# Performance work log

Measured on AMD Instinct MI355X. Metric: run time of the kernel, lower is better.

The kernel has to match this reference:

```python
import jax, jax.numpy as jnp
import numpy as np

N, T, S, E, H, DFF = 4, 2048, 2048, 512, 8, 2048
DH = E // H
EPS = 1e-5


def layer_norm(x, w, b):
    m = jnp.mean(x, axis=-1, keepdims=True)
    v = jnp.mean(jnp.square(x - m), axis=-1, keepdims=True)
    return (x - m) * jax.lax.rsqrt(v + EPS) * w + b


def mha(q, k, v, wq, bq, wk, bk, wv, bv, wo, bo, mask=None):
    # q: (N,Tq,E), k/v: (N,Tk,E); torch Linear convention: y = x @ W.T + b
    Nq, Tq, _ = q.shape
    Tk = k.shape[1]
    Q = (q @ wq.T + bq).reshape(Nq, Tq, H, DH).transpose(0, 2, 1, 3)  # (N,H,Tq,DH)
    K = (k @ wk.T + bk).reshape(Nq, Tk, H, DH).transpose(0, 2, 1, 3)
    V = (v @ wv.T + bv).reshape(Nq, Tk, H, DH).transpose(0, 2, 1, 3)
    scores = jnp.einsum('bhtd,bhsd->bhts', Q, K) * (1.0 / np.sqrt(DH))  # (N,H,Tq,Tk)
    if mask is not None:
        scores = jnp.where(mask, scores, jnp.float32(-1e9))
    attn = jax.nn.softmax(scores, axis=-1)
    out = jnp.einsum('bhts,bhsd->bhtd', attn, V)  # (N,H,Tq,DH)
    out = out.transpose(0, 2, 1, 3).reshape(Nq, Tq, E)
    return out @ wo.T + bo


def setup_inputs() -> dict:
    key = jax.random.key(0)
    ks = jax.random.split(key, 20)
    s = 0.02

    def lin(k, out_d, in_d):
        return jax.random.normal(k, (out_d, in_d), jnp.float32) * s

    inp = {
        'tgt': jax.random.normal(ks[0], (N, T, E), jnp.float32),
        'memory': jax.random.normal(ks[1], (N, S, E), jnp.float32),
        'tgt_mask': jnp.tril(jnp.ones((T, T), dtype=bool)),  # causal (T,T)
        # self-attention params
        'sa_wq': lin(ks[2], E, E), 'sa_bq': jnp.zeros((E,), jnp.float32),
        'sa_wk': lin(ks[3], E, E), 'sa_bk': jnp.zeros((E,), jnp.float32),
        'sa_wv': lin(ks[4], E, E), 'sa_bv': jnp.zeros((E,), jnp.float32),
        'sa_wo': lin(ks[5], E, E), 'sa_bo': jnp.zeros((E,), jnp.float32),
        # cross-attention params
        'ca_wq': lin(ks[6], E, E), 'ca_bq': jnp.zeros((E,), jnp.float32),
        'ca_wk': lin(ks[7], E, E), 'ca_bk': jnp.zeros((E,), jnp.float32),
        'ca_wv': lin(ks[8], E, E), 'ca_bv': jnp.zeros((E,), jnp.float32),
        'ca_wo': lin(ks[9], E, E), 'ca_bo': jnp.zeros((E,), jnp.float32),
        # FFN params
        'w1': lin(ks[10], DFF, E), 'b1': jnp.zeros((DFF,), jnp.float32),
        'w2': lin(ks[11], E, DFF), 'b2': jnp.zeros((E,), jnp.float32),
        # LayerNorm params
        'ln1_w': jnp.ones((E,), jnp.float32), 'ln1_b': jnp.zeros((E,), jnp.float32),
        'ln2_w': jnp.ones((E,), jnp.float32), 'ln2_b': jnp.zeros((E,), jnp.float32),
        'ln3_w': jnp.ones((E,), jnp.float32), 'ln3_b': jnp.zeros((E,), jnp.float32),
    }
    return inp


def reference(tgt, memory, tgt_mask,
              sa_wq, sa_bq, sa_wk, sa_bk, sa_wv, sa_bv, sa_wo, sa_bo,
              ca_wq, ca_bq, ca_wk, ca_bk, ca_wv, ca_bv, ca_wo, ca_bo,
              w1, b1, w2, b2,
              ln1_w, ln1_b, ln2_w, ln2_b, ln3_w, ln3_b):
    # stage 1: masked self-attention + residual + LN (dropout=0 / eval mode)
    sa = mha(tgt, tgt, tgt, sa_wq, sa_bq, sa_wk, sa_bk, sa_wv, sa_bv, sa_wo, sa_bo, mask=tgt_mask)
    x = layer_norm(tgt + sa, ln1_w, ln1_b)
    # stage 2: cross-attention over encoder memory + residual + LN
    ca = mha(x, memory, memory, ca_wq, ca_bq, ca_wk, ca_bk, ca_wv, ca_bv, ca_wo, ca_bo)
    x = layer_norm(x + ca, ln2_w, ln2_b)
    # stage 3: FFN (ReLU) + residual + LN
    mlp = jax.nn.relu(x @ w1.T + b1) @ w2.T + b2
    out = layer_norm(x + mlp, ln3_w, ln3_b)
    return out
```

## Files before the change

### kernel.cpp

```cpp
#include <hip/hip_runtime.h>
#include <hip/hip_bf16.h>
#include <cstdint>

typedef short short8 __attribute__((ext_vector_type(8)));
typedef short short4v __attribute__((ext_vector_type(4)));
typedef float f32x4 __attribute__((ext_vector_type(4)));
typedef float f32x16 __attribute__((ext_vector_type(16)));

#define GLL16(gp, lp) __builtin_amdgcn_global_load_lds( \
    (const __attribute__((address_space(1))) unsigned int*)(gp), \
    (__attribute__((address_space(3))) unsigned int*)(lp), 16, 0, 0)

__device__ __forceinline__ float bf2f(ushort u) {
    union { unsigned int i; float f; } v; v.i = ((unsigned int)u) << 16; return v.f;
}
__device__ __forceinline__ ushort f2bf(float f) {
    union { float f; unsigned int u; } v; v.f = f;
    unsigned int r = v.u + 0x7FFFu + ((v.u >> 16) & 1u);
    return (ushort)(r >> 16);
}
__device__ __forceinline__ int cvtpk_bf16(float lo, float hi) {
    int r;
    asm("v_cvt_pk_bf16_f32 %0, %1, %2" : "=v"(r) : "v"(lo), "v"(hi));
    return r;
}
__device__ __forceinline__ void plane32_swap(int& a, int& b) {
    asm volatile("v_permlane32_swap_b32 %0, %1" : "+v"(a), "+v"(b));
}

struct CvtArgs {
    const float* src[12];
    ushort*      dst[12];
};
__global__ __launch_bounds__(256) void f2b_all(CvtArgs a)
{
    int id = blockIdx.x;
    int seg, boff;
    if (id < 4096)       { seg = 0; boff = id; }
    else if (id < 8192)  { seg = 1; boff = id - 4096; }
    else if (id < 10240) { int t = id - 8192; seg = 2 + (t >> 8); boff = t & 255; }
    else if (id < 11264) { seg = 10; boff = id - 10240; }
    else                 { seg = 11; boff = id - 11264; }
    int i = (boff * 256 + threadIdx.x) * 4;
    f32x4 v = *(const f32x4*)(a.src[seg] + i);
    short4v o;
#pragma unroll
    for (int e = 0; e < 4; ++e) o[e] = (short)f2bf(v[e]);
    *(short4v*)(a.dst[seg] + i) = o;
}

template<int MODE, int DEPTH>
__global__ __launch_bounds__(256) void gemm_bt(
    const ushort* __restrict__ A, const ushort* __restrict__ W,
    const float* __restrict__ b0, const float* __restrict__ b1,
    const float* __restrict__ b2,
    ushort* __restrict__ C0, ushort* __restrict__ C1, ushort* __restrict__ C2,
    int M, int N, int K)
{
    __shared__ ushort As[DEPTH][128 * 32];
    __shared__ ushort Bs[DEPTH][128 * 32];
    const int tid = threadIdx.x;
    const int l  = tid & 63;
    const int w  = tid >> 6;
    const int wr = w >> 1, wc = w & 1;
    const int bn = blockIdx.x, bm = blockIdx.y;
    const int lg = l >> 4, li = l & 15;

    const ushort* Ab = A + (size_t)(bm * 128) * K;
    const ushort* Bb = W + (size_t)(bn * 128) * K;

    f32x4 acc[4][4] = {};

    const int r0 = tid >> 2,         s0 = (tid & 3) ^ ((r0 >> 2) & 3);
    const int r1 = (tid + 256) >> 2, s1 = (tid & 3) ^ ((r1 >> 2) & 3);

    auto stage = [&](int buf, int kt) {
        const ushort* Ak = Ab + kt * 32;
        const ushort* Bk = Bb + kt * 32;
        GLL16(Ak + (size_t)r0 * K + s0 * 8, &As[buf][tid * 8]);
        GLL16(Ak + (size_t)r1 * K + s1 * 8, &As[buf][(tid + 256) * 8]);
        GLL16(Bk + (size_t)r0 * K + s0 * 8, &Bs[buf][tid * 8]);
        GLL16(Bk + (size_t)r1 * K + s1 * 8, &Bs[buf][(tid + 256) * 8]);
    };

    const int nk = K >> 5;
#pragma unroll
    for (int p = 0; p < DEPTH - 1; ++p)
        if (p < nk) stage(p, p);

    for (int kt = 0; kt < nk; ++kt) {
        const int b = kt & (DEPTH - 1);
        const int nxt = kt + DEPTH - 1;
        if (nxt < nk) stage(nxt & (DEPTH - 1), nxt);
        const int rem = nk - 1 - kt;
        const int fl = rem < DEPTH - 1 ? rem : DEPTH - 1;
        if (fl >= 3)      asm volatile("s_waitcnt vmcnt(12)" ::: "memory");
        else if (fl == 2) asm volatile("s_waitcnt vmcnt(8)"  ::: "memory");
        else if (fl == 1) asm volatile("s_waitcnt vmcnt(4)"  ::: "memory");
        else              asm volatile("s_waitcnt vmcnt(0)"  ::: "memory");
        __builtin_amdgcn_s_barrier();
        __builtin_amdgcn_sched_barrier(0);

        short8 af[4], bfr[4];
#pragma unroll
        for (int mi = 0; mi < 4; ++mi) {
            int row = wr * 64 + mi * 16 + li;
            int ch  = lg ^ ((row >> 2) & 3);
            af[mi] = *(const short8*)(&As[b][row * 32 + ch * 8]);
        }
#pragma unroll
        for (int ni = 0; ni < 4; ++ni) {
            int row = wc * 64 + ni * 16 + li;
            int ch  = lg ^ ((row >> 2) & 3);
            bfr[ni] = *(const short8*)(&Bs[b][row * 32 + ch * 8]);
        }
#pragma unroll
        for (int mi = 0; mi < 4; ++mi)
#pragma unroll
            for (int ni = 0; ni < 4; ++ni)
                acc[mi][ni] = __builtin_amdgcn_mfma_f32_16x16x32_bf16(
                    af[mi], bfr[ni], acc[mi][ni], 0, 0, 0);

        __builtin_amdgcn_sched_barrier(0);
        asm volatile("s_waitcnt lgkmcnt(0)" ::: "memory");
        __builtin_amdgcn_s_barrier();
    }

    const int crow0 = bm * 128 + wr * 64 + lg * 4;
    const int ccol0 = bn * 128 + wc * 64 + li;
    const int sec = (MODE == 2 || MODE == 3) ? (bn >> 2) : 0;
    const float* bp = b0;
    ushort* Cw = C0;
    bool vsec = false;
    if (MODE == 2) {
        bp = (sec == 0) ? b0 : (sec == 1) ? b1 : b2;
        Cw = (sec == 0) ? C0 : (sec == 1) ? C1 : C2;
        vsec = (sec == 2);
    } else if (MODE == 3) {
        bp = (sec == 0) ? b0 : b1;
        Cw = (sec == 0) ? C0 : C1;
        vsec = (sec == 1);
    }
    const int Nout = (MODE == 2 || MODE == 3) ? 512 : N;

#pragma unroll
    for (int ni = 0; ni < 4; ++ni) {
        int col = ccol0 + ni * 16;
        int cl  = (MODE == 2 || MODE == 3) ? (col & 511) : col;
        float bv = bp[cl];
#pragma unroll
        for (int mi = 0; mi < 4; ++mi) {
            int row = crow0 + mi * 16;
            if (vsec) {
                int n = row >> 11, t = row & 2047;
                int h = cl >> 6,  d = cl & 63;
                size_t base = ((size_t)((n * 8 + h) * 64 + d)) * 2048 + t;
                short4v pk;
#pragma unroll
                for (int r = 0; r < 4; ++r) pk[r] = (short)f2bf(acc[mi][ni][r] + bv);
                *(short4v*)(Cw + base) = pk;
            } else {
#pragma unroll
                for (int r = 0; r < 4; ++r) {
                    float v = acc[mi][ni][r] + bv;
                    if (MODE == 1) v = fmaxf(v, 0.f);
                    Cw[(size_t)(row + r) * Nout + cl] = f2bf(v);
                }
            }
        }
    }
}

template<bool CAUSAL>
__global__ __launch_bounds__(512, 4) void attn_kernel(
    const ushort* __restrict__ Q, const ushort* __restrict__ K,
    const ushort* __restrict__ Vt, ushort* __restrict__ O, int Tk)
{
    __shared__ ushort SH[32768];
    const int tid = threadIdx.x;
    const int l = tid & 63, w = tid >> 6;
    const int ck = w >> 2, wq = w & 3;
    const int c = l & 31, hi = l >> 5;
    const int q0 = blockIdx.x * 128;
    const int nh = blockIdx.y, n = nh >> 3, h = nh & 7;
    const int qrow = q0 + wq * 32 + c;

    short8 qf[4];
#pragma unroll
    for (int s = 0; s < 4; ++s)
        qf[s] = *(const short8*)(Q + (size_t)(n * 2048 + qrow) * 512
                                   + h * 64 + s * 16 + hi * 8);

    f32x16 oacc[2] = {};
    float lsum = 0.f;

    const ushort* Kbase = K + (size_t)(n * 2048) * 512 + h * 64;
    const ushort* Vbase = Vt + (size_t)nh * 64 * Tk;

    const int t256 = tid & 255;
    const int rowA = t256 >> 3;
    const int csA  = (t256 & 7) ^ (rowA & 7);

    auto stage = [&](int buf, int j0) {
        ushort* kd = SH + (ck * 2 + buf) * 4096;
        ushort* vd = SH + 16384 + (ck * 2 + buf) * 4096;
        GLL16(Kbase + (size_t)(j0 + rowA) * 512 + csA * 8,      kd + t256 * 8);
        GLL16(Kbase + (size_t)(j0 + rowA + 32) * 512 + csA * 8, kd + (t256 + 256) * 8);
        GLL16(Vbase + (size_t)rowA * Tk + j0 + csA * 8,         vd + t256 * 8);
        GLL16(Vbase + (size_t)(rowA + 32) * Tk + j0 + csA * 8,  vd + (t256 + 256) * 8);
    };

    const float SC = 0.125f * 1.44269504f;
    const int cnt = CAUSAL ? ((int)blockIdx.x + 1) : (Tk >> 7);

    stage(0, ck * 64);
    for (int s = 0; s < cnt; ++s) {
        const int b  = s & 1;
        const int j0 = (ck + 2 * s) << 6;
        if (s + 1 < cnt) {
            stage(b ^ 1, j0 + 128);
            asm volatile("s_waitcnt vmcnt(4)" ::: "memory");
        } else {
            asm volatile("s_waitcnt vmcnt(0)" ::: "memory");
        }
        __builtin_amdgcn_s_barrier();
        __builtin_amdgcn_sched_barrier(0);

        const ushort* kls = SH + (ck * 2 + b) * 4096;
        const ushort* vls = SH + 16384 + (ck * 2 + b) * 4096;

        f32x16 sacc[2] = {};
        __builtin_amdgcn_s_setprio(1);
#pragma unroll
        for (int ks = 0; ks < 4; ++ks) {
#pragma unroll
            for (int t2 = 0; t2 < 2; ++t2) {
                int row = t2 * 32 + c;
                int ch  = (ks * 2 + hi) ^ (row & 7);
                short8 kf = *(const short8*)(kls + row * 64 + ch * 8);
                sacc[t2] = __builtin_amdgcn_mfma_f32_32x32x16_bf16(
                    kf, qf[ks], sacc[t2], 0, 0, 0);
            }
        }
        __builtin_amdgcn_s_setprio(0);

        const bool domask = CAUSAL && (j0 + 64 > q0);
#pragma unroll
        for (int t2 = 0; t2 < 2; ++t2) {
            float pv[16];
#pragma unroll
            for (int reg = 0; reg < 16; ++reg) {
                float p = exp2f(sacc[t2][reg] * SC);
                if (domask) {
                    int jg = j0 + t2 * 32 + (reg & 3) + 8 * (reg >> 2) + 4 * hi;
                    if (jg > qrow) p = 0.f;
                }
                lsum += p;
                pv[reg] = p;
            }
            int X0 = cvtpk_bf16(pv[0],  pv[1]),  Y0 = cvtpk_bf16(pv[2],  pv[3]);
            int X1 = cvtpk_bf16(pv[4],  pv[5]),  Y1 = cvtpk_bf16(pv[6],  pv[7]);
            int X2 = cvtpk_bf16(pv[8],  pv[9]),  Y2 = cvtpk_bf16(pv[10], pv[11]);
            int X3 = cvtpk_bf16(pv[12], pv[13]), Y3 = cvtpk_bf16(pv[14], pv[15]);
            plane32_swap(X0, X1); plane32_swap(Y0, Y1);
            plane32_swap(X2, X3); plane32_swap(Y2, Y3);
            union { int i[4]; short8 s; } pa0 = {{X0, Y0, X1, Y1}},
                                          pa1 = {{X2, Y2, X3, Y3}};
            __builtin_amdgcn_s_setprio(1);
#pragma unroll
            for (int sp = 0; sp < 2; ++sp) {
                short8 pa = sp ? pa1.s : pa0.s;
#pragma unroll
                for (int dc = 0; dc < 2; ++dc) {
                    int row = dc * 32 + c;
                    int ch  = (t2 * 4 + sp * 2 + hi) ^ (row & 7);
                    short8 vb = *(const short8*)(vls + row * 64 + ch * 8);
                    oacc[dc] = __builtin_amdgcn_mfma_f32_32x32x16_bf16(
                        pa, vb, oacc[dc], 0, 0, 0);
                }
            }
            __builtin_amdgcn_s_setprio(0);
        }

        __builtin_amdgcn_sched_barrier(0);
        asm volatile("s_waitcnt lgkmcnt(0)" ::: "memory");
        __builtin_amdgcn_s_barrier();
    }

    lsum += __shfl_xor(lsum, 32);

    float* m = (float*)SH;
    const int mbase = (wq * 64 + l) * 36;
    if (ck == 1) {
#pragma unroll
        for (int dc = 0; dc < 2; ++dc)
#pragma unroll
            for (int r4 = 0; r4 < 4; ++r4) {
                f32x4 v;
#pragma unroll
                for (int e = 0; e < 4; ++e) v[e] = oacc[dc][r4 * 4 + e];
                *(f32x4*)(m + mbase + dc * 16 + r4 * 4) = v;
            }
        m[mbase + 32] = lsum;
    }
    __syncthreads();
    if (ck == 0) {
#pragma unroll
        for (int dc = 0; dc < 2; ++dc)
#pragma unroll
            for (int r4 = 0; r4 < 4; ++r4) {
                f32x4 v = *(const f32x4*)(m + mbase + dc * 16 + r4 * 4);
#pragma unroll
                for (int e = 0; e < 4; ++e) oacc[dc][r4 * 4 + e] += v[e];
            }
        lsum += m[mbase + 32];
        float linv = 1.f / lsum;
#pragma unroll
        for (int dc = 0; dc < 2; ++dc)
#pragma unroll
            for (int reg = 0; reg < 16; ++reg) {
                int qloc = (reg & 3) + 8 * (reg >> 2) + 4 * hi;
                float lv = __shfl(linv, qloc);
                size_t off = (size_t)(n * 2048 + q0 + wq * 32 + qloc) * 512
                           + h * 64 + dc * 32 + c;
                O[off] = f2bf(oacc[dc][reg] * lv);
            }
    }
}

template<int F32OUT>
__global__ __launch_bounds__(256) void ln_kernel(
    const ushort* __restrict__ X, const ushort* __restrict__ Y,
    const float* __restrict__ W, const float* __restrict__ B,
    void* __restrict__ outp)
{
    const int row = blockIdx.x * 4 + (threadIdx.x >> 6);
    const int l = threadIdx.x & 63;
    const size_t off = (size_t)row * 512 + l * 8;
    short8 xv = *(const short8*)(X + off);
    short8 yv = *(const short8*)(Y + off);
    float v[8], s = 0.f, s2 = 0.f;
#pragma unroll
    for (int e = 0; e < 8; ++e) {
        float f = bf2f((ushort)xv[e]) + bf2f((ushort)yv[e]);
        v[e] = f; s += f; s2 += f * f;
    }
#pragma unroll
    for (int m = 1; m < 64; m <<= 1) {
        s  += __shfl_xor(s,  m);
        s2 += __shfl_xor(s2, m);
    }
    float mean = s * (1.f / 512.f);
    float var  = s2 * (1.f / 512.f) - mean * mean;
    float rs   = rsqrtf(var + 1e-5f);
    f32x4 w0 = *(const f32x4*)(W + l * 8);
    f32x4 w1 = *(const f32x4*)(W + l * 8 + 4);
    f32x4 b0 = *(const f32x4*)(B + l * 8);
    f32x4 b1 = *(const f32x4*)(B + l * 8 + 4);
    float wv[8] = {w0[0], w0[1], w0[2], w0[3], w1[0], w1[1], w1[2], w1[3]};
    float bv[8] = {b0[0], b0[1], b0[2], b0[3], b1[0], b1[1], b1[2], b1[3]};
    if (F32OUT) {
        float* out = (float*)outp;
#pragma unroll
        for (int e = 0; e < 8; ++e)
            out[off + e] = (v[e] - mean) * rs * wv[e] + bv[e];
    } else {
        ushort* out = (ushort*)outp;
        short8 ov;
#pragma unroll
        for (int e = 0; e < 8; ++e)
            ov[e] = (short)f2bf((v[e] - mean) * rs * wv[e] + bv[e]);
        *(short8*)(out + off) = ov;
    }
}

extern "C" void kernel_launch(void* const* d_in, const int* in_sizes, int n_in,
                              void* d_out, int out_size, void* d_ws, size_t ws_size,
                              hipStream_t stream)
{
    (void)in_sizes; (void)n_in; (void)out_size; (void)ws_size;
    const float* tgt  = (const float*)d_in[0];
    const float* mem  = (const float*)d_in[1];
    const float* sa_wq = (const float*)d_in[3];
    const float* sa_bq = (const float*)d_in[4];
    const float* sa_wk = (const float*)d_in[5];
    const float* sa_bk = (const float*)d_in[6];
    const float* sa_wv = (const float*)d_in[7];
    const float* sa_bv = (const float*)d_in[8];
    const float* sa_wo = (const float*)d_in[9];
    const float* sa_bo = (const float*)d_in[10];
    const float* ca_wq = (const float*)d_in[11];
    const float* ca_bq = (const float*)d_in[12];
    const float* ca_wk = (const float*)d_in[13];
    const float* ca_bk = (const float*)d_in[14];
    const float* ca_wv = (const float*)d_in[15];
    const float* ca_bv = (const float*)d_in[16];
    const float* ca_wo = (const float*)d_in[17];
    const float* ca_bo = (const float*)d_in[18];
    const float* w1    = (const float*)d_in[19];
    const float* b1    = (const float*)d_in[20];
    const float* w2    = (const float*)d_in[21];
    const float* b2    = (const float*)d_in[22];
    const float* ln1w  = (const float*)d_in[23];
    const float* ln1b  = (const float*)d_in[24];
    const float* ln2w  = (const float*)d_in[25];
    const float* ln2b  = (const float*)d_in[26];
    const float* ln3w  = (const float*)d_in[27];
    const float* ln3b  = (const float*)d_in[28];

    const size_t SE = (size_t)8192 * 512;
    const size_t EE = (size_t)512 * 512;
    ushort* ws = (ushort*)d_ws;
    ushort* Wb   = ws;
    ushort* bsqkv = Wb;
    ushort* bswo  = Wb + 3 * EE;
    ushort* bcwq  = Wb + 4 * EE;
    ushort* bckv  = Wb + 5 * EE;
    ushort* bcwo  = Wb + 7 * EE;
    ushort* bw1   = Wb + 8 * EE;
    ushort* bw2   = bw1 + 4 * EE;
    ushort* tgtb = Wb + 16 * EE;
    ushort* memb = tgtb + SE;
    ushort* Qb   = memb + SE;
    ushort* Kb   = Qb + SE;
    ushort* Vb   = Kb + SE;
    ushort* X1   = Vb + SE;
    ushort* AO   = X1 + SE;
    ushort* PO   = Qb;
    ushort* X2   = tgtb;
    ushort* Hb   = Qb;

    dim3 blk(256);
    dim3 blk512(512);
    dim3 gqkv(12, 64);
    dim3 gkv(8, 64);
    dim3 g512(4, 64);
    dim3 g2048(16, 64);
    dim3 ga(16, 32);
    dim3 gln(2048);

    CvtArgs ca;
    ca.src[0] = tgt;    ca.dst[0] = tgtb;
    ca.src[1] = mem;    ca.dst[1] = memb;
    ca.src[2] = sa_wq;  ca.dst[2] = bsqkv;
    ca.src[3] = sa_wk;  ca.dst[3] = bsqkv + EE;
    ca.src[4] = sa_wv;  ca.dst[4] = bsqkv + 2 * EE;
    ca.src[5] = sa_wo;  ca.dst[5] = bswo;
    ca.src[6] = ca_wq;  ca.dst[6] = bcwq;
    ca.src[7] = ca_wk;  ca.dst[7] = bckv;
    ca.src[8] = ca_wv;  ca.dst[8] = bckv + EE;
    ca.src[9] = ca_wo;  ca.dst[9] = bcwo;
    ca.src[10] = w1;    ca.dst[10] = bw1;
    ca.src[11] = w2;    ca.dst[11] = bw2;
    f2b_all<<<12288, blk, 0, stream>>>(ca);

    gemm_bt<2, 2><<<gqkv, blk, 0, stream>>>(tgtb, bsqkv, sa_bq, sa_bk, sa_bv,
                                            Qb, Kb, Vb, 8192, 1536, 512);
    attn_kernel<true><<<ga, blk512, 0, stream>>>(Qb, Kb, Vb, AO, 2048);
    gemm_bt<0, 4><<<g512, blk, 0, stream>>>(AO, bswo, sa_bo, nullptr, nullptr,
                                            PO, nullptr, nullptr, 8192, 512, 512);
    ln_kernel<0><<<gln, blk, 0, stream>>>(tgtb, PO, ln1w, ln1b, X1);

    gemm_bt<0, 4><<<g512, blk, 0, stream>>>(X1, bcwq, ca_bq, nullptr, nullptr,
                                            Qb, nullptr, nullptr, 8192, 512, 512);
    gemm_bt<3, 2><<<gkv, blk, 0, stream>>>(memb, bckv, ca_bk, ca_bv, nullptr,
                                           Kb, Vb, nullptr, 8192, 1024, 512);
    attn_kernel<false><<<ga, blk512, 0, stream>>>(Qb, Kb, Vb, AO, 2048);
    gemm_bt<0, 4><<<g512, blk, 0, stream>>>(AO, bcwo, ca_bo, nullptr, nullptr,
                                            PO, nullptr, nullptr, 8192, 512, 512);
    ln_kernel<0><<<gln, blk, 0, stream>>>(X1, PO, ln2w, ln2b, X2);

    gemm_bt<1, 2><<<g2048, blk, 0, stream>>>(X2, bw1, b1, nullptr, nullptr,
                                             Hb, nullptr, nullptr, 8192, 2048, 512);
    gemm_bt<0, 4><<<g512, blk, 0, stream>>>(Hb, bw2, b2, nullptr, nullptr,
                                            AO, nullptr, nullptr, 8192, 512, 2048);
    ln_kernel<1><<<gln, blk, 0, stream>>>(X2, AO, ln3w, ln3b, d_out);
}
```

Baseline: 312.9 us.

## Split attention KV halves into separate blocks and merge partials in a kernel

After: 308.4 us. Within noise of the previous version (-1.4%).

```diff
diff --git a/kernel.cpp b/kernel.cpp
--- a/kernel.cpp
+++ b/kernel.cpp
@@ -172,17 +172,28 @@
 }
 
 template<bool CAUSAL>
-__global__ __launch_bounds__(512, 4) void attn_kernel(
+__global__ __launch_bounds__(256) void attn_kernel(
     const ushort* __restrict__ Q, const ushort* __restrict__ K,
-    const ushort* __restrict__ Vt, ushort* __restrict__ O, int Tk)
-{
-    __shared__ ushort SH[32768];
+    const ushort* __restrict__ Vt, ushort* __restrict__ P0,
+    ushort* __restrict__ P1, float* __restrict__ Ls, int Tk)
+{
+    __shared__ ushort SH[16384];
     const int tid = threadIdx.x;
-    const int l = tid & 63, w = tid >> 6;
-    const int ck = w >> 2, wq = w & 3;
+    const int l = tid & 63, wq = tid >> 6;
     const int c = l & 31, hi = l >> 5;
-    const int q0 = blockIdx.x * 128;
-    const int nh = blockIdx.y, n = nh >> 3, h = nh & 7;
+
+    int qt, nh, ck;
+    if (CAUSAL) {
+        int g = (int)blockIdx.x >> 6;
+        qt = (g < 8) ? (15 - g) : (g - 8);
+        int r = blockIdx.x & 63;
+        nh = r >> 1; ck = r & 1;
+    } else {
+        int pos = ((int)blockIdx.x & 7) * 128 + ((int)blockIdx.x >> 3);
+        nh = pos >> 5; ck = (pos >> 4) & 1; qt = pos & 15;
+    }
+    const int q0 = qt * 128;
+    const int n = nh >> 3, h = nh & 7;
     const int qrow = q0 + wq * 32 + c;
 
     short8 qf[4];
@@ -197,21 +208,20 @@
     const ushort* Kbase = K + (size_t)(n * 2048) * 512 + h * 64;
     const ushort* Vbase = Vt + (size_t)nh * 64 * Tk;
 
-    const int t256 = tid & 255;
-    const int rowA = t256 >> 3;
-    const int csA  = (t256 & 7) ^ (rowA & 7);
+    const int rowA = tid >> 3;
+    const int csA  = (tid & 7) ^ (rowA & 7);
 
     auto stage = [&](int buf, int j0) {
-        ushort* kd = SH + (ck * 2 + buf) * 4096;
-        ushort* vd = SH + 16384 + (ck * 2 + buf) * 4096;
-        GLL16(Kbase + (size_t)(j0 + rowA) * 512 + csA * 8,      kd + t256 * 8);
-        GLL16(Kbase + (size_t)(j0 + rowA + 32) * 512 + csA * 8, kd + (t256 + 256) * 8);
-        GLL16(Vbase + (size_t)rowA * Tk + j0 + csA * 8,         vd + t256 * 8);
-        GLL16(Vbase + (size_t)(rowA + 32) * Tk + j0 + csA * 8,  vd + (t256 + 256) * 8);
+        ushort* kd = SH + buf * 4096;
+        ushort* vd = SH + 8192 + buf * 4096;
+        GLL16(Kbase + (size_t)(j0 + rowA) * 512 + csA * 8,      kd + tid * 8);
+        GLL16(Kbase + (size_t)(j0 + rowA + 32) * 512 + csA * 8, kd + (tid + 256) * 8);
+        GLL16(Vbase + (size_t)rowA * Tk + j0 + csA * 8,         vd + tid * 8);
+        GLL16(Vbase + (size_t)(rowA + 32) * Tk + j0 + csA * 8,  vd + (tid + 256) * 8);
     };
 
     const float SC = 0.125f * 1.44269504f;
-    const int cnt = CAUSAL ? ((int)blockIdx.x + 1) : (Tk >> 7);
+    const int cnt = CAUSAL ? (qt + 1) : (Tk >> 7);
 
     stage(0, ck * 64);
     for (int s = 0; s < cnt; ++s) {
@@ -226,8 +236,8 @@
         __builtin_amdgcn_s_barrier();
         __builtin_amdgcn_sched_barrier(0);
 
-        const ushort* kls = SH + (ck * 2 + b) * 4096;
-        const ushort* vls = SH + 16384 + (ck * 2 + b) * 4096;
+        const ushort* kls = SH + b * 4096;
+        const ushort* vls = SH + 8192 + b * 4096;
 
         f32x16 sacc[2] = {};
         __builtin_amdgcn_s_setprio(1);
@@ -289,43 +299,37 @@
 
     lsum += __shfl_xor(lsum, 32);
 
-    float* m = (float*)SH;
-    const int mbase = (wq * 64 + l) * 36;
-    if (ck == 1) {
-#pragma unroll
-        for (int dc = 0; dc < 2; ++dc)
-#pragma unroll
-            for (int r4 = 0; r4 < 4; ++r4) {
-                f32x4 v;
-#pragma unroll
-                for (int e = 0; e < 4; ++e) v[e] = oacc[dc][r4 * 4 + e];
-                *(f32x4*)(m + mbase + dc * 16 + r4 * 4) = v;
-            }
-        m[mbase + 32] = lsum;
-    }
-    __syncthreads();
-    if (ck == 0) {
-#pragma unroll
-        for (int dc = 0; dc < 2; ++dc)
-#pragma unroll
-            for (int r4 = 0; r4 < 4; ++r4) {
-                f32x4 v = *(const f32x4*)(m + mbase + dc * 16 + r4 * 4);
-#pragma unroll
-                for (int e = 0; e < 4; ++e) oacc[dc][r4 * 4 + e] += v[e];
-            }
-        lsum += m[mbase + 32];
-        float linv = 1.f / lsum;
-#pragma unroll
-        for (int dc = 0; dc < 2; ++dc)
-#pragma unroll
-            for (int reg = 0; reg < 16; ++reg) {
-                int qloc = (reg & 3) + 8 * (reg >> 2) + 4 * hi;
-                float lv = __shfl(linv, qloc);
-                size_t off = (size_t)(n * 2048 + q0 + wq * 32 + qloc) * 512
-                           + h * 64 + dc * 32 + c;
-                O[off] = f2bf(oacc[dc][reg] * lv);
-            }
-    }
+    ushort* Pw = ck ? P1 : P0;
+    if (hi == 0)
+        Ls[ck * 65536 + nh * 2048 + q0 + wq * 32 + c] = lsum;
+#pragma unroll
+    for (int dc = 0; dc < 2; ++dc)
+#pragma unroll
+        for (int reg = 0; reg < 16; ++reg) {
+            int qloc = (reg & 3) + 8 * (reg >> 2) + 4 * hi;
+            size_t off = (size_t)(n * 2048 + q0 + wq * 32 + qloc) * 512
+                       + h * 64 + dc * 32 + c;
+            Pw[off] = f2bf(oacc[dc][reg]);
+        }
+}
+
+__global__ __launch_bounds__(256) void attn_merge(
+    const ushort* __restrict__ P0, const ushort* __restrict__ P1,
+    const float* __restrict__ Ls, ushort* __restrict__ out)
+{
+    const int row = blockIdx.x * 4 + (threadIdx.x >> 6);
+    const int l = threadIdx.x & 63;
+    const size_t off = (size_t)row * 512 + l * 8;
+    const int n = row >> 11, q = row & 2047, h = l >> 3;
+    const int lidx = (n * 8 + h) * 2048 + q;
+    float linv = 1.f / (Ls[lidx] + Ls[65536 + lidx]);
+    short8 a = *(const short8*)(P0 + off);
+    short8 b = *(const short8*)(P1 + off);
+    short8 o;
+#pragma unroll
+    for (int e = 0; e < 8; ++e)
+        o[e] = (short)f2bf((bf2f((ushort)a[e]) + bf2f((ushort)b[e])) * linv);
+    *(short8*)(out + off) = o;
 }
 
 template<int F32OUT>
@@ -426,17 +430,17 @@
     ushort* Vb   = Kb + SE;
     ushort* X1   = Vb + SE;
     ushort* AO   = X1 + SE;
+    float*  LsBuf = (float*)(AO + SE);
     ushort* PO   = Qb;
     ushort* X2   = tgtb;
     ushort* Hb   = Qb;
 
     dim3 blk(256);
-    dim3 blk512(512);
     dim3 gqkv(12, 64);
     dim3 gkv(8, 64);
     dim3 g512(4, 64);
     dim3 g2048(16, 64);
-    dim3 ga(16, 32);
+    dim3 ga(1024);
     dim3 gln(2048);
 
     CvtArgs ca;
@@ -456,7 +460,8 @@
 
     gemm_bt<2, 2><<<gqkv, blk, 0, stream>>>(tgtb, bsqkv, sa_bq, sa_bk, sa_bv,
                                             Qb, Kb, Vb, 8192, 1536, 512);
-    attn_kernel<true><<<ga, blk512, 0, stream>>>(Qb, Kb, Vb, AO, 2048);
+    attn_kernel<true><<<ga, blk, 0, stream>>>(Qb, Kb, Vb, AO, X1, LsBuf, 2048);
+    attn_merge<<<gln, blk, 0, stream>>>(AO, X1, LsBuf, AO);
     gemm_bt<0, 4><<<g512, blk, 0, stream>>>(AO, bswo, sa_bo, nullptr, nullptr,
                                             PO, nullptr, nullptr, 8192, 512, 512);
     ln_kernel<0><<<gln, blk, 0, stream>>>(tgtb, PO, ln1w, ln1b, X1);
@@ -465,7 +470,8 @@
                                             Qb, nullptr, nullptr, 8192, 512, 512);
     gemm_bt<3, 2><<<gkv, blk, 0, stream>>>(memb, bckv, ca_bk, ca_bv, nullptr,
                                            Kb, Vb, nullptr, 8192, 1024, 512);
-    attn_kernel<false><<<ga, blk512, 0, stream>>>(Qb, Kb, Vb, AO, 2048);
+    attn_kernel<false><<<ga, blk, 0, stream>>>(Qb, Kb, Vb, AO, tgtb, LsBuf, 2048);
+    attn_merge<<<gln, blk, 0, stream>>>(AO, tgtb, LsBuf, AO);
     gemm_bt<0, 4><<<g512, blk, 0, stream>>>(AO, bcwo, ca_bo, nullptr, nullptr,
                                             PO, nullptr, nullptr, 8192, 512, 512);
     ln_kernel<0><<<gln, blk, 0, stream>>>(X1, PO, ln2w, ln2b, X2);
```
